# Performance work log

Measured on AMD Instinct MI355X. Metric: run time of the kernel, lower is better.

Reference implementation:

```python
import jax, jax.numpy as jnp
import numpy as np

TEMP = 0.1
EPS = 1e-12  # F.normalize eps


def setup_inputs() -> dict:
    key = jax.random.key(0)
    k1, k2 = jax.random.split(key)
    B, C, N = 8, 128, 4096
    features = jax.random.normal(k1, (B, C, N), dtype=jnp.float32)
    labels_all = jax.random.randint(k2, (B, N), 0, 16, dtype=jnp.int32)
    return {"features": features, "labels_all": labels_all}


def _per_cloud_loss(features_map, labels):
    # features_map: [C, N], labels: [N]
    v = features_map.T  # [N, C]
    v = v / jnp.maximum(jnp.linalg.norm(v, axis=1, keepdims=True), EPS)
    dp = jnp.exp(jnp.matmul(v, v.T) / TEMP)  # [N, N]
    n = dp.shape[0]
    # remove diagonal (dot_products - diag(diagonal))
    dp = dp * (1.0 - jnp.eye(n, dtype=dp.dtype))
    mask = labels[:, None] == labels[None, :]  # [N, N]
    positives = jnp.sum(jnp.where(mask, dp, 0.0), axis=1)
    negatives = jnp.sum(jnp.where(mask, 0.0, dp), axis=1)
    deviation = -jnp.log(positives / (positives + negatives))
    return jnp.mean(deviation)


def reference(features, labels_all):
    # features: [B, C, N], labels_all: [B, N]
    losses = jax.vmap(_per_cloud_loss)(features, labels_all)  # [B]
    return jnp.mean(losses)
```

## Files before the change

### kernel.cpp

```cpp
#include <hip/hip_runtime.h>
#include <hip/hip_bf16.h>
#include <math.h>

#define BATCH 8
#define NPTS 4096
#define CH 128
#define CTG 4
#define CHUNK 32
#define NCHUNK (NPTS / (CTG * CHUNK))
#define NBUF 4

#define SQRT_TEMP_LOG2E 3.79828256f

typedef __attribute__((ext_vector_type(4))) float f32x4;
typedef __attribute__((ext_vector_type(4))) int   i32x4;
typedef __attribute__((ext_vector_type(8))) short bf16x8;

typedef __attribute__((address_space(3))) unsigned int lds_uint;
typedef __attribute__((address_space(1))) const unsigned int gbl_uint;

__device__ __forceinline__ void load_lds16(const void* g, const void* l) {
    __builtin_amdgcn_global_load_lds((gbl_uint*)g, (lds_uint*)l, 16, 0, 0);
}

__device__ __forceinline__ float fast_exp2(float x) {
    return __builtin_amdgcn_exp2f(x);
}

__global__ __launch_bounds__(256) void normalize_kernel(
    const float* __restrict__ f, __hip_bfloat16* __restrict__ vn,
    float* __restrict__ pos, float* __restrict__ neg, float* __restrict__ out)
{
    int idx = blockIdx.x * 256 + threadIdx.x;
    int pp = idx >> 2, q = idx & 3;
    int b = pp >> 11, n2 = (pp & 2047) * 2;
    const float* base = f + (size_t)b * CH * NPTS + (size_t)(q * 32) * NPTS + n2;

    float x0[32], x1[32];
    float s0 = 0.0f, s1 = 0.0f;
    #pragma unroll
    for (int c = 0; c < 32; c++) {
        float2 v = *(const float2*)(base + (size_t)c * NPTS);
        x0[c] = v.x; x1[c] = v.y;
        s0 += v.x * v.x; s1 += v.y * v.y;
    }
    s0 += __shfl_xor(s0, 1); s0 += __shfl_xor(s0, 2);
    s1 += __shfl_xor(s1, 1); s1 += __shfl_xor(s1, 2);
    float sc0 = SQRT_TEMP_LOG2E / fmaxf(sqrtf(s0), 1e-12f);
    float sc1 = SQRT_TEMP_LOG2E / fmaxf(sqrtf(s1), 1e-12f);

    int point = b * NPTS + n2;
    __hip_bfloat16* o0 = vn + (size_t)point * CH + q * 32;
    #pragma unroll
    for (int c0 = 0; c0 < 32; c0 += 8) {
        union { __hip_bfloat16 h[8]; uint4 u; } pk;
        #pragma unroll
        for (int j = 0; j < 8; j++) pk.h[j] = __float2bfloat16(x0[c0 + j] * sc0);
        *((uint4*)(o0 + c0)) = pk.u;
    }
    __hip_bfloat16* o1 = o0 + CH;
    #pragma unroll
    for (int c0 = 0; c0 < 32; c0 += 8) {
        union { __hip_bfloat16 h[8]; uint4 u; } pk;
        #pragma unroll
        for (int j = 0; j < 8; j++) pk.h[j] = __float2bfloat16(x1[c0 + j] * sc1);
        *((uint4*)(o1 + c0)) = pk.u;
    }
    if (q == 0)      { pos[point] = 0.0f; pos[point + 1] = 0.0f; }
    else if (q == 1) { neg[point] = 0.0f; neg[point + 1] = 0.0f; }
    if (idx == 0) out[0] = 0.0f;
}

__global__ __launch_bounds__(256, 4) void tile_kernel(
    const __hip_bfloat16* __restrict__ vn, const int* __restrict__ labels,
    float* __restrict__ pos, float* __restrict__ neg)
{
    __shared__ short lB[NBUF][CHUNK * CH];
    __shared__ int labL[NPTS / CTG];

    const int ctg = blockIdx.x, rt = blockIdx.y, b = blockIdx.z;
    const int tid = threadIdx.x;
    const int w = tid >> 6, lane = tid & 63;
    const int lane15 = lane & 15, quad = lane >> 4;

    const int row0 = rt * 128;
    const int colbase = ctg * (NPTS / CTG);
    const __hip_bfloat16* vb = vn + (size_t)b * NPTS * CH;
    const int* labb = labels + b * NPTS;

    auto stage = [&](int buf, int chunk) {
        const __hip_bfloat16* Bb = vb + (size_t)(colbase + chunk * CHUNK) * CH;
        #pragma unroll
        for (int i = 0; i < 2; i++) {
            int ldsrow = w * 8 + i * 4;
            int r = ldsrow + quad;
            int g = lane15 ^ (r & 15);
            load_lds16(Bb + (size_t)r * CH + g * 8, &lB[buf][ldsrow * CH]);
        }
    };

    load_lds16(labb + colbase + w * 256 + lane * 4, &labL[w * 256]);

    bf16x8 afrag[2][4];
    int lr[2];
    #pragma unroll
    for (int mi = 0; mi < 2; mi++) {
        const int row_l = w * 32 + mi * 16 + lane15;
        const __hip_bfloat16* Arow = vb + (size_t)(row0 + row_l) * CH;
        #pragma unroll
        for (int ks = 0; ks < 4; ks++)
            afrag[mi][ks] = *(const bf16x8*)(Arow + (ks * 4 + quad) * 8);
        lr[mi] = labb[row0 + row_l];
    }

    stage(0, 0);
    stage(1, 1);
    stage(2, 2);

    int vad[2][4];
    #pragma unroll
    for (int ni = 0; ni < 2; ni++)
        #pragma unroll
        for (int ks = 0; ks < 4; ks++)
            vad[ni][ks] = (((ni * 16 + lane15) * CH) +
                           (((ks * 4 + quad) ^ lane15) << 3)) * 2;

    float pacc[2] = {0.0f, 0.0f}, tacc[2] = {0.0f, 0.0f};
    const f32x4 zf = {0.0f, 0.0f, 0.0f, 0.0f};
    f32x4 accA[2][2], accB[2][2];

#define MFMA_PH(BUF_, ACC_)                                                   \
    {                                                                         \
        _Pragma("unroll")                                                     \
        for (int ni = 0; ni < 2; ni++) {                                      \
            bf16x8 bf = *(const bf16x8*)((const char*)(&lB[0][0]) +           \
                         (BUF_) * (CHUNK * CH * 2) + vad[ni][0]);             \
            ACC_[0][ni] = __builtin_amdgcn_mfma_f32_16x16x32_bf16(            \
                bf, afrag[0][0], zf, 0, 0, 0);                                \
            ACC_[1][ni] = __builtin_amdgcn_mfma_f32_16x16x32_bf16(            \
                bf, afrag[1][0], zf, 0, 0, 0);                                \
        }                                                                     \
        _Pragma("unroll")                                                     \
        for (int ks = 1; ks < 4; ks++) {                                      \
            _Pragma("unroll")                                                 \
            for (int ni = 0; ni < 2; ni++) {                                  \
                bf16x8 bf = *(const bf16x8*)((const char*)(&lB[0][0]) +       \
                             (BUF_) * (CHUNK * CH * 2) + vad[ni][ks]);        \
                ACC_[0][ni] = __builtin_amdgcn_mfma_f32_16x16x32_bf16(        \
                    bf, afrag[0][ks], ACC_[0][ni], 0, 0, 0);                  \
                ACC_[1][ni] = __builtin_amdgcn_mfma_f32_16x16x32_bf16(        \
                    bf, afrag[1][ks], ACC_[1][ni], 0, 0, 0);                  \
            }                                                                 \
        }                                                                     \
    }

#define EPI_PH(EC_, ACC_)                                                     \
    {                                                                         \
        _Pragma("unroll")                                                     \
        for (int ni = 0; ni < 2; ni++) {                                      \
            const i32x4 lc = *(const i32x4*)&labL[(EC_) * CHUNK + ni * 16 +   \
                                                  quad * 4];                  \
            const int colblk = colbase + (EC_) * CHUNK + ni * 16;             \
            _Pragma("unroll")                                                 \
            for (int mi = 0; mi < 2; mi++) {                                  \
                const bool dblk = (colblk == row0 + w * 32 + mi * 16);        \
                if (dblk) {                                                   \
                    _Pragma("unroll")                                         \
                    for (int r = 0; r < 4; r++) {                             \
                        float e = fast_exp2(ACC_[mi][ni][r]);                 \
                        if (lane15 == quad * 4 + r) e = 0.0f;   \
                        tacc[mi] += e;                                        \
                        pacc[mi] += (lc[r] == lr[mi]) ? e : 0.0f;             \
                    }                                                         \
                } else {                                                      \
                    _Pragma("unroll")                                         \
                    for (int r = 0; r < 4; r++) {                             \
                        float e = fast_exp2(ACC_[mi][ni][r]);                 \
                        tacc[mi] += e;                                        \
                        pacc[mi] += (lc[r] == lr[mi]) ? e : 0.0f;             \
                    }                                                         \
                }                                                             \
            }                                                                 \
        }                                                                     \
    }

#define BODY(C_, BUF_, CUR_, PRV_, DOEPI_)                                    \
    {                                                                         \
        __builtin_amdgcn_s_barrier();                                         \
        __builtin_amdgcn_s_setprio(1);                                        \
        MFMA_PH(BUF_, CUR_);                                                  \
        stage(((BUF_) + 3) & 3, ((C_) + 3) & (NCHUNK - 1));                   \
        if (DOEPI_) { EPI_PH((C_) - 1, PRV_); }                               \
        __builtin_amdgcn_s_setprio(0);                                        \
        asm volatile("s_waitcnt vmcnt(4)" ::: "memory");                      \
    }

    asm volatile("s_waitcnt vmcnt(4)" ::: "memory");
    BODY(0, 0, accA, accB, 0);
    #pragma unroll 1
    for (int c = 1; c < 29; c += 4) {
        BODY(c + 0, 1, accB, accA, 1);
        BODY(c + 1, 2, accA, accB, 1);
        BODY(c + 2, 3, accB, accA, 1);
        BODY(c + 3, 0, accA, accB, 1);
    }
    BODY(29, 1, accB, accA, 1);
    BODY(30, 2, accA, accB, 1);
    __builtin_amdgcn_s_barrier();
    __builtin_amdgcn_s_setprio(1);
    MFMA_PH(3, accB);
    EPI_PH(30, accA);
    __builtin_amdgcn_s_setprio(0);
    EPI_PH(31, accB);

#undef BODY
#undef EPI_PH
#undef MFMA_PH

    #pragma unroll
    for (int mi = 0; mi < 2; mi++) {
        float p = pacc[mi], tt = tacc[mi];
        p  += __shfl_xor(p, 16);   p  += __shfl_xor(p, 32);
        tt += __shfl_xor(tt, 16);  tt += __shfl_xor(tt, 32);
        if (lane < 16) {
            const int row_l = w * 32 + mi * 16 + lane15;
            atomicAdd(&pos[b * NPTS + row0 + row_l], p);
            atomicAdd(&neg[b * NPTS + row0 + row_l], tt - p);
        }
    }
}

__global__ __launch_bounds__(256) void finalize_kernel(
    const float* __restrict__ pos, const float* __restrict__ neg,
    float* __restrict__ out)
{
    int base = blockIdx.x * 1024 + threadIdx.x;
    float acc = 0.0f;
    #pragma unroll
    for (int k = 0; k < 4; k++) {
        int i = base + k * 256;
        float p = pos[i];
        float t = p + neg[i];
        acc += __logf(t / p);
    }
    #pragma unroll
    for (int off = 32; off; off >>= 1) acc += __shfl_down(acc, off);
    __shared__ float red[4];
    if ((threadIdx.x & 63) == 0) red[threadIdx.x >> 6] = acc;
    __syncthreads();
    if (threadIdx.x == 0) {
        float v = red[0] + red[1] + red[2] + red[3];
        atomicAdd(out, v * (1.0f / (BATCH * NPTS)));
    }
}

extern "C" void kernel_launch(void* const* d_in, const int* in_sizes, int n_in,
                              void* d_out, int out_size, void* d_ws, size_t ws_size,
                              hipStream_t stream)
{
    const float* features = (const float*)d_in[0];
    const int*   labels   = (const int*)d_in[1];
    float*       out      = (float*)d_out;

    __hip_bfloat16* vn = (__hip_bfloat16*)d_ws;
    float* pos = (float*)((char*)d_ws + (size_t)BATCH * NPTS * CH * sizeof(__hip_bfloat16));
    float* neg = pos + BATCH * NPTS;

    hipLaunchKernelGGL(normalize_kernel, dim3(BATCH * NPTS * 2 / 256), dim3(256), 0, stream,
                       features, vn, pos, neg, out);
    hipLaunchKernelGGL(tile_kernel, dim3(CTG, 32, BATCH), dim3(256), 0, stream,
                       vn, labels, pos, neg);
    hipLaunchKernelGGL(finalize_kernel, dim3(32), dim3(256), 0, stream, pos, neg, out);
}
```

Measured before the change: 116.0 us.

## Accumulate per-label exp sums with fp16 one-hot MFMA instead of scalar adds

The epilogue now converts the exp values to fp16 and multiplies them by a one-hot label matrix in a 16x16x16 fp16 MFMA. This gives per-row sums for each of the 16 labels, and the positive and total sums are picked out at the end, with diagonal terms subtracted separately. It moves the per-element compare/select/add work onto the matrix unit, but exp values are rounded to fp16, which could overflow or lose precision since exp(1/T) is about 22026. The normalize kernel also goes back to one point per thread, which doubles its grid and uses scalar instead of float2 loads.

```diff
diff --git a/kernel.cpp b/kernel.cpp
--- a/kernel.cpp
+++ b/kernel.cpp
@@ -12,9 +12,10 @@
 
 #define SQRT_TEMP_LOG2E 3.79828256f
 
-typedef __attribute__((ext_vector_type(4))) float f32x4;
-typedef __attribute__((ext_vector_type(4))) int   i32x4;
-typedef __attribute__((ext_vector_type(8))) short bf16x8;
+typedef __attribute__((ext_vector_type(4))) float    f32x4;
+typedef __attribute__((ext_vector_type(4))) int      i32x4;
+typedef __attribute__((ext_vector_type(8))) short    bf16x8;
+typedef __attribute__((ext_vector_type(4))) _Float16 f16x4;
 
 typedef __attribute__((address_space(3))) unsigned int lds_uint;
 typedef __attribute__((address_space(1))) const unsigned int gbl_uint;
@@ -25,6 +26,17 @@
 
 __device__ __forceinline__ float fast_exp2(float x) {
     return __builtin_amdgcn_exp2f(x);
+}
+
+__device__ __forceinline__ f32x4 mfma16(f16x4 a, f16x4 b, f32x4 c) {
+#if __has_builtin(__builtin_amdgcn_mfma_f32_16x16x16f16)
+    return __builtin_amdgcn_mfma_f32_16x16x16f16(a, b, c, 0, 0, 0);
+#else
+    f32x4 d = c;
+    asm volatile("v_mfma_f32_16x16x16_f16 %0, %1, %2, %0"
+                 : "+v"(d) : "v"(a), "v"(b));
+    return d;
+#endif
 }
 
 __global__ __launch_bounds__(256) void normalize_kernel(
@@ -32,42 +44,32 @@
     float* __restrict__ pos, float* __restrict__ neg, float* __restrict__ out)
 {
     int idx = blockIdx.x * 256 + threadIdx.x;
-    int pp = idx >> 2, q = idx & 3;
-    int b = pp >> 11, n2 = (pp & 2047) * 2;
-    const float* base = f + (size_t)b * CH * NPTS + (size_t)(q * 32) * NPTS + n2;
-
-    float x0[32], x1[32];
-    float s0 = 0.0f, s1 = 0.0f;
+    int point = idx >> 2, q = idx & 3;
+    int b = point >> 12, n = point & (NPTS - 1);
+    const float* base = f + (size_t)b * CH * NPTS + (size_t)(q * 32) * NPTS + n;
+
+    float x[32];
+    float ss = 0.0f;
     #pragma unroll
     for (int c = 0; c < 32; c++) {
-        float2 v = *(const float2*)(base + (size_t)c * NPTS);
-        x0[c] = v.x; x1[c] = v.y;
-        s0 += v.x * v.x; s1 += v.y * v.y;
-    }
-    s0 += __shfl_xor(s0, 1); s0 += __shfl_xor(s0, 2);
-    s1 += __shfl_xor(s1, 1); s1 += __shfl_xor(s1, 2);
-    float sc0 = SQRT_TEMP_LOG2E / fmaxf(sqrtf(s0), 1e-12f);
-    float sc1 = SQRT_TEMP_LOG2E / fmaxf(sqrtf(s1), 1e-12f);
-
-    int point = b * NPTS + n2;
-    __hip_bfloat16* o0 = vn + (size_t)point * CH + q * 32;
+        x[c] = base[(size_t)c * NPTS];
+        ss += x[c] * x[c];
+    }
+    ss += __shfl_xor(ss, 1);
+    ss += __shfl_xor(ss, 2);
+    float scale = SQRT_TEMP_LOG2E / fmaxf(sqrtf(ss), 1e-12f);
+
+    __hip_bfloat16* outp = vn + (size_t)point * CH + q * 32;
     #pragma unroll
     for (int c0 = 0; c0 < 32; c0 += 8) {
         union { __hip_bfloat16 h[8]; uint4 u; } pk;
         #pragma unroll
-        for (int j = 0; j < 8; j++) pk.h[j] = __float2bfloat16(x0[c0 + j] * sc0);
-        *((uint4*)(o0 + c0)) = pk.u;
-    }
-    __hip_bfloat16* o1 = o0 + CH;
-    #pragma unroll
-    for (int c0 = 0; c0 < 32; c0 += 8) {
-        union { __hip_bfloat16 h[8]; uint4 u; } pk;
-        #pragma unroll
-        for (int j = 0; j < 8; j++) pk.h[j] = __float2bfloat16(x1[c0 + j] * sc1);
-        *((uint4*)(o1 + c0)) = pk.u;
-    }
-    if (q == 0)      { pos[point] = 0.0f; pos[point + 1] = 0.0f; }
-    else if (q == 1) { neg[point] = 0.0f; neg[point + 1] = 0.0f; }
+        for (int j = 0; j < 8; j++)
+            pk.h[j] = __float2bfloat16(x[c0 + j] * scale);
+        *((uint4*)(outp + c0)) = pk.u;
+    }
+    if (q == 0) pos[point] = 0.0f;
+    else if (q == 1) neg[point] = 0.0f;
     if (idx == 0) out[0] = 0.0f;
 }
 
@@ -125,7 +127,8 @@
             vad[ni][ks] = (((ni * 16 + lane15) * CH) +
                            (((ks * 4 + quad) ^ lane15) << 3)) * 2;
 
-    float pacc[2] = {0.0f, 0.0f}, tacc[2] = {0.0f, 0.0f};
+    f32x4 qout[2] = {{0.0f, 0.0f, 0.0f, 0.0f}, {0.0f, 0.0f, 0.0f, 0.0f}};
+    float ddiag[2] = {0.0f, 0.0f};
     const f32x4 zf = {0.0f, 0.0f, 0.0f, 0.0f};
     f32x4 accA[2][2], accB[2][2];
 
@@ -160,26 +163,24 @@
         for (int ni = 0; ni < 2; ni++) {                                      \
             const i32x4 lc = *(const i32x4*)&labL[(EC_) * CHUNK + ni * 16 +   \
                                                   quad * 4];                  \
+            f16x4 oh;                                                         \
+            _Pragma("unroll")                                                 \
+            for (int j = 0; j < 4; j++)                                       \
+                oh[j] = (lc[j] == lane15) ? (_Float16)1.0f : (_Float16)0.0f;  \
             const int colblk = colbase + (EC_) * CHUNK + ni * 16;             \
             _Pragma("unroll")                                                 \
             for (int mi = 0; mi < 2; mi++) {                                  \
-                const bool dblk = (colblk == row0 + w * 32 + mi * 16);        \
-                if (dblk) {                                                   \
+                f16x4 eh;                                                     \
+                _Pragma("unroll")                                             \
+                for (int r = 0; r < 4; r++)                                   \
+                    eh[r] = (_Float16)fast_exp2(ACC_[mi][ni][r]);             \
+                if (colblk == row0 + w * 32 + mi * 16) {    \
                     _Pragma("unroll")                                         \
-                    for (int r = 0; r < 4; r++) {                             \
-                        float e = fast_exp2(ACC_[mi][ni][r]);                 \
-                        if (lane15 == quad * 4 + r) e = 0.0f;   \
-                        tacc[mi] += e;                                        \
-                        pacc[mi] += (lc[r] == lr[mi]) ? e : 0.0f;             \
-                    }                                                         \
-                } else {                                                      \
-                    _Pragma("unroll")                                         \
-                    for (int r = 0; r < 4; r++) {                             \
-                        float e = fast_exp2(ACC_[mi][ni][r]);                 \
-                        tacc[mi] += e;                                        \
-                        pacc[mi] += (lc[r] == lr[mi]) ? e : 0.0f;             \
-                    }                                                         \
+                    for (int r = 0; r < 4; r++)                               \
+                        if (lane15 == quad * 4 + r)                           \
+                            ddiag[mi] += (float)eh[r];                        \
                 }                                                             \
+                qout[mi] = mfma16(oh, eh, qout[mi]);                          \
             }                                                                 \
         }                                                                     \
     }
@@ -219,7 +220,13 @@
 
     #pragma unroll
     for (int mi = 0; mi < 2; mi++) {
-        float p = pacc[mi], tt = tacc[mi];
+        float p = -ddiag[mi], tt = -ddiag[mi];
+        #pragma unroll
+        for (int r = 0; r < 4; r++) {
+            float v = qout[mi][r];
+            tt += v;
+            p  += (quad * 4 + r == lr[mi]) ? v : 0.0f;
+        }
         p  += __shfl_xor(p, 16);   p  += __shfl_xor(p, 32);
         tt += __shfl_xor(tt, 16);  tt += __shfl_xor(tt, 32);
         if (lane < 16) {
@@ -266,7 +273,7 @@
     float* pos = (float*)((char*)d_ws + (size_t)BATCH * NPTS * CH * sizeof(__hip_bfloat16));
     float* neg = pos + BATCH * NPTS;
 
-    hipLaunchKernelGGL(normalize_kernel, dim3(BATCH * NPTS * 2 / 256), dim3(256), 0, stream,
+    hipLaunchKernelGGL(normalize_kernel, dim3(BATCH * NPTS * 4 / 256), dim3(256), 0, stream,
                        features, vn, pos, neg, out);
     hipLaunchKernelGGL(tile_kernel, dim3(CTG, 32, BATCH), dim3(256), 0, stream,
                        vn, labels, pos, neg);
```

Measured after the change: 111.9 us. -3.5%, faster.
